# Performance work log

Measured on AMD Instinct MI355X. Metric: run time of the kernel, lower is better.

The kernel has to match this reference:

```python
import jax, jax.numpy as jnp
import numpy as np

T = 512          # tokens
H = 2048         # hidden_size
E = 256          # n_routed_experts (8 groups x 32)
G = 8            # tucker groups
EPG = 32         # experts per group
K = 6            # top_k
I = 1408         # moe_intermediate_size
R1 = 128         # tucker input rank
R2 = 128         # tucker output rank


def setup_inputs() -> dict:
    key = jax.random.key(0)
    ks = jax.random.split(key, 12)
    s = 0.02
    return {
        "hidden_states": jax.random.normal(ks[0], (T, H), jnp.float32),
        "w_router": jax.random.normal(ks[1], (H, E), jnp.float32) * s,
        # gate_proj Tucker factors: H -> I
        "U_in_gate": jax.random.normal(ks[2], (G, H, R1), jnp.float32) * s,
        "core_gate": jax.random.normal(ks[3], (E, R1, R2), jnp.float32) * s,
        "U_out_gate": jax.random.normal(ks[4], (G, I, R2), jnp.float32) * s,
        # up_proj Tucker factors: H -> I
        "U_in_up": jax.random.normal(ks[5], (G, H, R1), jnp.float32) * s,
        "core_up": jax.random.normal(ks[6], (E, R1, R2), jnp.float32) * s,
        "U_out_up": jax.random.normal(ks[7], (G, I, R2), jnp.float32) * s,
        # down_proj Tucker factors: I -> H
        "U_in_down": jax.random.normal(ks[8], (G, I, R1), jnp.float32) * s,
        "core_down": jax.random.normal(ks[9], (E, R1, R2), jnp.float32) * s,
        "U_out_down": jax.random.normal(ks[10], (G, H, R2), jnp.float32) * s,
    }


def _tucker_apply(x, g, e, U_in, core, U_out):
    """Per-expert Tucker linear: y_t = ((x_t @ U_in[g_t]) @ core[e_t]) @ U_out[g_t].T
    x: [Td, din]; g: [Td] group ids; e: [Td] full expert ids.
    U_in: [G, din, r1]; core: [E, r1, r2]; U_out: [G, dout, r2]."""
    h1 = jnp.einsum('td,gdr->tgr', x, U_in)                       # [Td, G, r1]
    h1 = jnp.take_along_axis(h1, g[:, None, None], axis=1)[:, 0]  # [Td, r1]
    h2 = jnp.einsum('tr,trs->ts', h1, core[e])                    # [Td, r2]
    y = jnp.einsum('ts,gds->tgd', h2, U_out)                      # [Td, G, dout]
    return jnp.take_along_axis(y, g[:, None, None], axis=1)[:, 0]


def reference(hidden_states, w_router, U_in_gate, core_gate, U_out_gate,
              U_in_up, core_up, U_out_up, U_in_down, core_down, U_out_down):
    n_tok, hid = hidden_states.shape
    router_logits = hidden_states @ w_router                          # [T, E]
    probs = jax.nn.softmax(router_logits.astype(jnp.float32), axis=-1)
    routing_weights, selected = jax.lax.top_k(probs, K)               # [T, K]
    routing_weights = routing_weights / routing_weights.sum(-1, keepdims=True)
    routing_weights = routing_weights.astype(hidden_states.dtype)

    xd = jnp.repeat(hidden_states, K, axis=0)                         # [T*K, H]
    e = selected.reshape(-1)                                          # [T*K]
    g = e // EPG                                                      # group ids

    gate_out = _tucker_apply(xd, g, e, U_in_gate, core_gate, U_out_gate)
    up_out = _tucker_apply(xd, g, e, U_in_up, core_up, U_out_up)
    inter = jax.nn.silu(gate_out) * up_out                            # [T*K, I]
    down_out = _tucker_apply(inter, g, e, U_in_down, core_down, U_out_down)

    combined = (down_out.reshape(n_tok, K, hid) * routing_weights[..., None]).sum(axis=1)
    return combined
```

## Files before the change

kernel.cpp:

```cpp
#include <hip/hip_runtime.h>
#include <cmath>
#include <cstdint>

#define TNUM 512
#define HID 2048
#define NEXP 256
#define NGRP 8
#define KTOP 6
#define IDIM 1408
#define RNK 128
#define NPAIR (TNUM*KTOP)
#define NRCAP 3328
#define MAXTILES (NRCAP/32)

typedef _Float16 f16;
typedef f16  f16x8 __attribute__((ext_vector_type(8)));
typedef f16  f16x4 __attribute__((ext_vector_type(4)));
typedef float f32x4 __attribute__((ext_vector_type(4)));
#define MFMA16(a,b,c) __builtin_amdgcn_mfma_f32_16x16x32_f16((a),(b),(c),0,0,0)

static __device__ __forceinline__ float4 ld4(const float* p){ return *reinterpret_cast<const float4*>(p); }
static __device__ __forceinline__ void st4(float* p, float4 v){ *reinterpret_cast<float4*>(p) = v; }
static __device__ __forceinline__ f16x8 ldh8(const f16* p){ return *reinterpret_cast<const f16x8*>(p); }

constexpr size_t A256(size_t x){ return (x + 255) & ~(size_t)255; }
constexpr size_t OFF_SEL    = 0;
constexpr size_t OFF_WT     = A256(OFF_SEL    + (size_t)NPAIR*4);
constexpr size_t OFF_CNT    = A256(OFF_WT     + (size_t)NPAIR*4);
constexpr size_t OFF_ESTART = A256(OFF_CNT    + (size_t)NEXP*4);
constexpr size_t OFF_TG     = A256(OFF_ESTART + (size_t)NEXP*4);
constexpr size_t OFF_HDR    = A256(OFF_TG     + (size_t)MAXTILES*4);
constexpr size_t OFF_ROWT   = A256(OFF_HDR    + 16);
constexpr size_t OFF_POS    = A256(OFF_ROWT   + (size_t)NRCAP*4);
constexpr size_t OFF_BIG    = A256(OFF_POS    + (size_t)NPAIR*4);

constexpr size_t SZ_XH    = (size_t)TNUM*HID*2;
constexpr size_t SZ_UTI   = (size_t)NGRP*RNK*HID*2;
constexpr size_t SZ_CT    = (size_t)NEXP*RNK*RNK*2;
constexpr size_t SZ_H1ALL = (size_t)2*TNUM*NGRP*RNK*2;
constexpr size_t SZ_UO    = (size_t)NGRP*IDIM*RNK*2;
constexpr size_t SZ_UOD   = (size_t)NGRP*HID*RNK*2;
constexpr size_t SZ_WR    = (size_t)NEXP*HID*2;
constexpr size_t SZ_H2    = (size_t)NRCAP*RNK*2;
constexpr size_t SZ_INTER = (size_t)NRCAP*IDIM*2;
constexpr size_t SZ_DOWNO = (size_t)NRCAP*HID*4;

constexpr size_t OFF_XH    = OFF_BIG;
constexpr size_t OFF_XL    = OFF_XH   + SZ_XH;
constexpr size_t OFF_UTIG  = OFF_XL   + SZ_XH;
constexpr size_t OFF_UTIU  = OFF_UTIG + SZ_UTI;
constexpr size_t OFF_CGT   = OFF_UTIU + SZ_UTI;
constexpr size_t OFF_CUT   = OFF_CGT  + SZ_CT;
constexpr size_t OFF_H1    = OFF_CUT  + SZ_CT;
constexpr size_t REG_END   = OFF_H1   + SZ_H1ALL;
constexpr size_t OFF_INTER = OFF_XH;
constexpr size_t OFF_DOWNO = OFF_XH;
constexpr size_t OFF_LPART = OFF_H1;
constexpr size_t OFF_UOG   = REG_END;
constexpr size_t OFF_UOU   = OFF_UOG  + SZ_UO;
constexpr size_t OFF_UTID  = OFF_UOU  + SZ_UO;
constexpr size_t OFF_UOD   = OFF_UTID + SZ_UO;
constexpr size_t OFF_CDT   = OFF_UOD  + SZ_UOD;
constexpr size_t OFF_WRH   = OFF_CDT  + SZ_CT;
constexpr size_t OFF_WRL   = OFF_WRH  + SZ_WR;
constexpr size_t OFF_H2G   = OFF_WRL  + SZ_WR;
constexpr size_t OFF_H2U   = OFF_H2G  + SZ_H2;
constexpr size_t OFF_D1    = OFF_H2U  + SZ_H2;
constexpr size_t OFF_D2    = OFF_D1   + SZ_H2;
constexpr size_t WS_NEED   = OFF_D2   + SZ_H2;
static_assert(OFF_INTER + SZ_INTER <= OFF_CGT, "inter overlay must end before cores");
static_assert(OFF_DOWNO + SZ_DOWNO <= OFF_UOG, "downo overlay must end before persistent tail");

__global__ __launch_bounds__(256) void k_cvt_main(
    const float* __restrict__ x,   const float* __restrict__ Uog,
    const float* __restrict__ Uou, const float* __restrict__ Uod,
    const float* __restrict__ wr,
    f16* __restrict__ xh, f16* __restrict__ xl,
    f16* __restrict__ uog, f16* __restrict__ uou, f16* __restrict__ uod,
    f16* __restrict__ wh, f16* __restrict__ wl,
    int* __restrict__ cnt){
  __shared__ float tile[32][33];
  const int b = blockIdx.x, tid = threadIdx.x;
  if(b < 1024){
    const size_t i = (size_t)b*256 + tid;
    float4 v = ld4(x + i*4);
    f16x4 H, L;
    H[0]=(f16)v.x; L[0]=(f16)(v.x-(float)H[0]);
    H[1]=(f16)v.y; L[1]=(f16)(v.y-(float)H[1]);
    H[2]=(f16)v.z; L[2]=(f16)(v.z-(float)H[2]);
    H[3]=(f16)v.w; L[3]=(f16)(v.w-(float)H[3]);
    *reinterpret_cast<f16x4*>(xh + i*4) = H;
    *reinterpret_cast<f16x4*>(xl + i*4) = L;
    return;
  }
  if(b < 5888){
    const float* in; f16* hi; size_t i;
    if(b < 2432){        in = Uog; hi = uog; i = (size_t)(b-1024)*256 + tid; }
    else if(b < 3840){   in = Uou; hi = uou; i = (size_t)(b-2432)*256 + tid; }
    else {               in = Uod; hi = uod; i = (size_t)(b-3840)*256 + tid; }
    float4 v = ld4(in + i*4);
    f16x4 H;
    H[0]=(f16)(v.x*16.f); H[1]=(f16)(v.y*16.f); H[2]=(f16)(v.z*16.f); H[3]=(f16)(v.w*16.f);
    *reinterpret_cast<f16x4*>(hi + i*4) = H;
    return;
  }
  const int wb = b - 5888;
  if(wb == 0) cnt[tid] = 0;
  const int c0 = (wb & 7)*32, r0 = (wb >> 3)*32;
  { const int r = tid>>3, c4 = (tid&7)*4;
    float4 v = ld4(wr + (size_t)(r0+r)*NEXP + c0 + c4);
    tile[r][c4]=v.x; tile[r][c4+1]=v.y; tile[r][c4+2]=v.z; tile[r][c4+3]=v.w; }
  __syncthreads();
  { const int c = tid>>3, r4 = (tid&7)*4;
    f16x4 H, L;
    #pragma unroll
    for(int k = 0; k < 4; k++){
      float v = tile[r4+k][c]*16.f;
      H[k] = (f16)v; L[k] = (f16)(v - (float)H[k]);
    }
    const size_t o = (size_t)(c0+c)*HID + r0 + r4;
    *reinterpret_cast<f16x4*>(wh + o) = H;
    *reinterpret_cast<f16x4*>(wl + o) = L; }
}

__global__ __launch_bounds__(256) void k_cvt_t(
    const float* __restrict__ Uig, const float* __restrict__ Uiu, const float* __restrict__ Uid,
    const float* __restrict__ cg,  const float* __restrict__ cu,  const float* __restrict__ cd,
    f16* __restrict__ ig, f16* __restrict__ iu, f16* __restrict__ idn,
    f16* __restrict__ cgt, f16* __restrict__ cut, f16* __restrict__ cdt){
  __shared__ float tile[32][33];
  const int b = blockIdx.x, tid = threadIdx.x;
  const float* in; f16* o; int r0, c0, R, OR;
  if(b < 6144){
    const int cx = b & 3, ry = (b>>2) & 63, z = b >> 8;
    const int tensor = z >> 3, g = z & 7;
    if(tensor == 0){ in = Uig; o = ig; R = HID; }
    else if(tensor == 1){ in = Uiu; o = iu; R = HID; }
    else { in = Uid; o = idn; R = IDIM; }
    r0 = ry*32; c0 = cx*32;
    if(r0 >= R) return;
    in += (size_t)g*R*RNK; o += (size_t)g*RNK*R;
    OR = R;
  } else {
    const int cb = b - 6144;
    const int tensor = cb >> 12, rem = cb & 4095, e = rem >> 4;
    if(tensor == 0){ in = cg; o = cgt; }
    else if(tensor == 1){ in = cu; o = cut; }
    else { in = cd; o = cdt; }
    in += (size_t)e*RNK*RNK; o += (size_t)e*RNK*RNK;
    r0 = ((rem>>2)&3)*32; c0 = (rem&3)*32; R = RNK; OR = RNK;
  }
  { const int r = tid>>3, c4 = (tid&7)*4;
    float4 v = ld4(in + (size_t)(r0+r)*RNK + c0 + c4);
    tile[r][c4]=v.x; tile[r][c4+1]=v.y; tile[r][c4+2]=v.z; tile[r][c4+3]=v.w; }
  __syncthreads();
  { const int c = tid>>3, r4 = (tid&7)*4;
    f16x4 H;
    #pragma unroll
    for(int k = 0; k < 4; k++) H[k] = (f16)(tile[r4+k][c]*16.f);
    *reinterpret_cast<f16x4*>(o + (size_t)(c0+c)*OR + r0 + r4) = H; }
}

__global__ __launch_bounds__(256) void k_router_mfma(
    const f16* __restrict__ xh, const f16* __restrict__ xl,
    const f16* __restrict__ wh, const f16* __restrict__ wl,
    float* __restrict__ lpart){
  __shared__ float red[4][32][64];
  const int m = blockIdx.x, ecol = blockIdx.y, kz = blockIdx.z;
  const int tid = threadIdx.x;
  const int wid = tid>>6, lane = tid&63, q = lane>>4, id = lane&15;
  const int r0 = m*32, e0 = ecol*64;
  const int kb = kz*512 + wid*128;
  f32x4 acc[2][4];
  #pragma unroll
  for(int f = 0; f < 2; f++)
    #pragma unroll
    for(int c = 0; c < 4; c++) acc[f][c] = (f32x4){0.f,0.f,0.f,0.f};
  #pragma unroll
  for(int kk = 0; kk < 128; kk += 32){
    const size_t a0 = (size_t)(r0+id)*HID    + kb + kk + q*8;
    const size_t a1 = (size_t)(r0+16+id)*HID + kb + kk + q*8;
    f16x8 ah0 = ldh8(xh + a0), al0 = ldh8(xl + a0);
    f16x8 ah1 = ldh8(xh + a1), al1 = ldh8(xl + a1);
    #pragma unroll
    for(int c = 0; c < 4; c++){
      const size_t bo = (size_t)(e0 + c*16 + id)*HID + kb + kk + q*8;
      f16x8 bh = ldh8(wh + bo);
      f16x8 bl = ldh8(wl + bo);
      acc[0][c] = MFMA16(ah0, bh, acc[0][c]);
      acc[0][c] = MFMA16(ah0, bl, acc[0][c]);
      acc[0][c] = MFMA16(al0, bh, acc[0][c]);
      acc[1][c] = MFMA16(ah1, bh, acc[1][c]);
      acc[1][c] = MFMA16(ah1, bl, acc[1][c]);
      acc[1][c] = MFMA16(al1, bh, acc[1][c]);
    }
  }
  #pragma unroll
  for(int f = 0; f < 2; f++)
    #pragma unroll
    for(int c = 0; c < 4; c++)
      #pragma unroll
      for(int r = 0; r < 4; r++)
        red[wid][f*16 + q*4 + r][c*16 + id] = acc[f][c][r];
  __syncthreads();
  const int row = tid>>3, c8 = (tid&7)*8;
  float o[8];
  #pragma unroll
  for(int j = 0; j < 8; j++)
    o[j] = (red[0][row][c8+j] + red[1][row][c8+j] + red[2][row][c8+j] + red[3][row][c8+j])*0.0625f;
  float* dst = &lpart[((size_t)kz*TNUM + r0 + row)*NEXP + e0 + c8];
  st4(dst,     make_float4(o[0],o[1],o[2],o[3]));
  st4(dst + 4, make_float4(o[4],o[5],o[6],o[7]));
}

__global__ __launch_bounds__(256) void k_topk(const float* __restrict__ lpart,
                                              int* __restrict__ sel,
                                              float* __restrict__ wt,
                                              int* __restrict__ cnt){
  __shared__ float wv[4];
  __shared__ int   wi[4];
  __shared__ float swin[KTOP];
  __shared__ int   iwin[KTOP];
  const int t = blockIdx.x, tid = threadIdx.x;
  const int lane = tid & 63, wid = tid >> 6;
  const size_t base = (size_t)t*NEXP + tid;
  float v = lpart[base] + lpart[base + (size_t)TNUM*NEXP]
          + lpart[base + (size_t)2*TNUM*NEXP] + lpart[base + (size_t)3*TNUM*NEXP];
  for(int k = 0; k < KTOP; k++){
    float cv = v; int ci = tid;
    #pragma unroll
    for(int off = 1; off < 64; off <<= 1){
      float ov = __shfl_xor(cv, off);
      int   oi = __shfl_xor(ci, off);
      if(ov > cv || (ov == cv && oi < ci)){ cv = ov; ci = oi; }
    }
    if(lane == 0){ wv[wid] = cv; wi[wid] = ci; }
    __syncthreads();
    if(tid == 0){
      float bv = wv[0]; int bi = wi[0];
      #pragma unroll
      for(int w2 = 1; w2 < 4; w2++)
        if(wv[w2] > bv || (wv[w2] == bv && wi[w2] < bi)){ bv = wv[w2]; bi = wi[w2]; }
      swin[k] = bv; iwin[k] = bi;
    }
    __syncthreads();
    if(tid == iwin[k]) v = -INFINITY;
  }
  if(tid == 0){
    float mx = swin[0], s = 0.f, ww[KTOP];
    #pragma unroll
    for(int k = 0; k < KTOP; k++){ ww[k] = expf(swin[k]-mx); s += ww[k]; }
    float inv = 1.f/s;
    #pragma unroll
    for(int k = 0; k < KTOP; k++){
      sel[t*KTOP+k] = iwin[k];
      wt[t*KTOP+k]  = ww[k]*inv;
      atomicAdd(&cnt[iwin[k]], 1);
    }
  }
}

__global__ __launch_bounds__(256) void k_meta_scatter(
    const int* __restrict__ cnt, const int* __restrict__ sel,
    int* __restrict__ estart, int* __restrict__ tile_group, int* __restrict__ hdr,
    int* __restrict__ row_t, int* __restrict__ pos_of_pair){
  __shared__ int scnt[256];
  __shared__ int gsum[8];
  __shared__ int g0[9];
  __shared__ int curs[256];
  const int tid = threadIdx.x;
  scnt[tid] = cnt[tid];
  if(tid < 8) gsum[tid] = 0;
  __syncthreads();
  atomicAdd(&gsum[tid>>5], scnt[tid]);
  __syncthreads();
  if(tid == 0){
    int run = 0;
    for(int g = 0; g < 8; g++){ g0[g] = run; run += (gsum[g]+31) & ~31; }
    g0[8] = run; hdr[0] = run>>5; hdr[1] = run;
  }
  __syncthreads();
  int g = tid >> 5, s = g0[g];
  for(int i = (g<<5); i < tid; i++) s += scnt[i];
  estart[tid] = s; curs[tid] = s;
  const int nt = g0[8] >> 5;
  for(int t2 = tid; t2 < MAXTILES; t2 += 256){
    int gg = -1;
    if(t2 < nt){
      for(int g2 = 0; g2 < 8; g2++) if(t2*32 >= g0[g2] && t2*32 < g0[g2+1]) gg = g2;
    }
    tile_group[t2] = gg;
  }
  __syncthreads();
  for(int p = tid; p < NPAIR; p += 256){
    const int e = sel[p];
    const int pos = atomicAdd(&curs[e], 1);
    row_t[pos] = p / KTOP;
    pos_of_pair[p] = pos;
  }
}

__global__ __launch_bounds__(256) void k_mm_stage1(
    const f16* __restrict__ xh,
    const f16* __restrict__ Bg_, const f16* __restrict__ Bu_,
    f16* __restrict__ H1){
  __shared__ float red[4][32][64];
  const int m = blockIdx.x, nt = blockIdx.y;
  const int pu = nt>>4, g = (nt>>1)&7, ch = nt&1;
  const f16* B = (pu ? Bu_ : Bg_) + (size_t)g*RNK*HID + (size_t)ch*64*HID;
  const int tid = threadIdx.x;
  const int wid = tid>>6, lane = tid&63, q = lane>>4, id = lane&15;
  const int kb = wid*512;
  const int r0 = m*32;
  f32x4 acc[2][4];
  #pragma unroll
  for(int f = 0; f < 2; f++)
    #pragma unroll
    for(int c = 0; c < 4; c++) acc[f][c] = (f32x4){0.f,0.f,0.f,0.f};
  #pragma unroll 4
  for(int kk = 0; kk < 512; kk += 32){
    f16x8 a0 = ldh8(xh + (size_t)(r0+id)*HID    + kb + kk + q*8);
    f16x8 a1 = ldh8(xh + (size_t)(r0+16+id)*HID + kb + kk + q*8);
    #pragma unroll
    for(int c = 0; c < 4; c++){
      f16x8 b = ldh8(B + (size_t)(c*16+id)*HID + kb + kk + q*8);
      acc[0][c] = MFMA16(a0, b, acc[0][c]);
      acc[1][c] = MFMA16(a1, b, acc[1][c]);
    }
  }
  #pragma unroll
  for(int f = 0; f < 2; f++)
    #pragma unroll
    for(int c = 0; c < 4; c++)
      #pragma unroll
      for(int r = 0; r < 4; r++)
        red[wid][f*16 + q*4 + r][c*16 + id] = acc[f][c][r];
  __syncthreads();
  f16* out = H1 + (size_t)pu*TNUM*(NGRP*RNK);
  const int row = tid>>3, c8 = (tid&7)*8;
  f16x8 o8;
  #pragma unroll
  for(int j = 0; j < 8; j++)
    o8[j] = (f16)(red[0][row][c8+j] + red[1][row][c8+j] + red[2][row][c8+j] + red[3][row][c8+j]);
  *reinterpret_cast<f16x8*>(&out[(size_t)(r0+row)*(NGRP*RNK) + g*RNK + ch*64 + c8]) = o8;
}

__global__ __launch_bounds__(256) void k_core2(
    const f16* __restrict__ Cg, const f16* __restrict__ Cu,
    const f16* __restrict__ H1,
    const int* __restrict__ estart, const int* __restrict__ cnt,
    const int* __restrict__ row_t,
    f16* __restrict__ h2g, f16* __restrict__ h2u){
  const int e = blockIdx.x, up = blockIdx.y;
  const int n = cnt[e];
  if(n == 0) return;
  const int j0 = estart[e], g = e >> 5;
  const f16* C = (up ? Cu : Cg) + (size_t)e*RNK*RNK;
  const f16* A = H1 + (size_t)up*TNUM*(NGRP*RNK);
  f16* o = up ? h2u : h2g;
  const int tid = threadIdx.x;
  const int wid = tid>>6, lane = tid&63, q = lane>>4, id = lane&15;
  for(int rt = 0; rt*16 < n; rt++){
    const int jrow = j0 + rt*16 + id;
    const int jj = jrow < j0+n ? jrow : j0;
    const f16* arow = A + (size_t)row_t[jj]*(NGRP*RNK) + g*RNK;
    f32x4 acc0 = (f32x4){0.f,0.f,0.f,0.f};
    f32x4 acc1 = (f32x4){0.f,0.f,0.f,0.f};
    #pragma unroll
    for(int kk = 0; kk < RNK; kk += 32){
      f16x8 a = ldh8(arow + kk + q*8);
      f16x8 b0 = ldh8(C + (size_t)(wid*32 + id)*RNK      + kk + q*8);
      f16x8 b1 = ldh8(C + (size_t)(wid*32 + 16 + id)*RNK + kk + q*8);
      acc0 = MFMA16(a, b0, acc0);
      acc1 = MFMA16(a, b1, acc1);
    }
    #pragma unroll
    for(int r = 0; r < 4; r++){
      const int j = j0 + rt*16 + q*4 + r;
      if(j < j0+n){
        o[(size_t)j*RNK + wid*32 + id]      = (f16)acc0[r];
        o[(size_t)j*RNK + wid*32 + 16 + id] = (f16)acc1[r];
      }
    }
  }
}

__global__ __launch_bounds__(128) void k_mm_gateup(
    const f16* __restrict__ Ag, const f16* __restrict__ Au,
    const f16* __restrict__ Bg, const f16* __restrict__ Bu,
    const int* __restrict__ tg,
    f16* __restrict__ inter){
  const int g = tg[blockIdx.x];
  if(g < 0) return;
  const int j0 = blockIdx.x*32;
  const int tid = threadIdx.x;
  const int wid = tid>>6, lane = tid&63, q = lane>>4, id = lane&15;
  const int c0 = blockIdx.y*128 + wid*64;
  const size_t bbase = (size_t)g*IDIM*RNK;
  f32x4 accg[2][4], accu[2][4];
  #pragma unroll
  for(int f = 0; f < 2; f++)
    #pragma unroll
    for(int c = 0; c < 4; c++){ accg[f][c] = (f32x4){0.f,0.f,0.f,0.f}; accu[f][c] = (f32x4){0.f,0.f,0.f,0.f}; }
  #pragma unroll 2
  for(int kk = 0; kk < RNK; kk += 32){
    const size_t a0off = (size_t)(j0+id)*RNK    + kk + q*8;
    const size_t a1off = (size_t)(j0+16+id)*RNK + kk + q*8;
    f16x8 ag0 = ldh8(Ag + a0off), ag1 = ldh8(Ag + a1off);
    f16x8 au0 = ldh8(Au + a0off), au1 = ldh8(Au + a1off);
    #pragma unroll
    for(int c = 0; c < 4; c++){
      const size_t boff = bbase + (size_t)(c0 + c*16 + id)*RNK + kk + q*8;
      f16x8 bg = ldh8(Bg + boff);
      f16x8 bu = ldh8(Bu + boff);
      accg[0][c] = MFMA16(ag0, bg, accg[0][c]);
      accg[1][c] = MFMA16(ag1, bg, accg[1][c]);
      accu[0][c] = MFMA16(au0, bu, accu[0][c]);
      accu[1][c] = MFMA16(au1, bu, accu[1][c]);
    }
  }
  #pragma unroll
  for(int f = 0; f < 2; f++)
    #pragma unroll
    for(int c = 0; c < 4; c++)
      #pragma unroll
      for(int r = 0; r < 4; r++){
        float vg = accg[f][c][r] * (1.f/4096.f);
        float vu = accu[f][c][r] * (1.f/4096.f);
        float sv = vg/(1.f+expf(-vg))*vu*256.f;
        inter[(size_t)(j0 + f*16 + q*4 + r)*IDIM + c0 + c*16 + id] = (f16)sv;
      }
}

__global__ __launch_bounds__(256) void k_mm_down_in(
    const f16* __restrict__ A_, const f16* __restrict__ B_,
    const int* __restrict__ tg,
    f16* __restrict__ d1){
  __shared__ float red[4][32][64];
  const int g = tg[blockIdx.x];
  if(g < 0) return;
  const int j0 = blockIdx.x*32;
  const int ch = blockIdx.y;
  const f16* B = B_ + (size_t)g*RNK*IDIM + (size_t)ch*64*IDIM;
  const int tid = threadIdx.x;
  const int wid = tid>>6, lane = tid&63, q = lane>>4, id = lane&15;
  const int kb = wid*352;
  f32x4 acc[2][4];
  #pragma unroll
  for(int f = 0; f < 2; f++)
    #pragma unroll
    for(int c = 0; c < 4; c++) acc[f][c] = (f32x4){0.f,0.f,0.f,0.f};
  #pragma unroll 2
  for(int kk = 0; kk < 352; kk += 32){
    f16x8 a0 = ldh8(A_ + (size_t)(j0+id)*IDIM    + kb + kk + q*8);
    f16x8 a1 = ldh8(A_ + (size_t)(j0+16+id)*IDIM + kb + kk + q*8);
    #pragma unroll
    for(int c = 0; c < 4; c++){
      f16x8 b = ldh8(B + (size_t)(c*16+id)*IDIM + kb + kk + q*8);
      acc[0][c] = MFMA16(a0, b, acc[0][c]);
      acc[1][c] = MFMA16(a1, b, acc[1][c]);
    }
  }
  #pragma unroll
  for(int f = 0; f < 2; f++)
    #pragma unroll
    for(int c = 0; c < 4; c++)
      #pragma unroll
      for(int r = 0; r < 4; r++)
        red[wid][f*16 + q*4 + r][c*16 + id] = acc[f][c][r];
  __syncthreads();
  const int row = tid>>3, c8 = (tid&7)*8;
  f16x8 o8;
  #pragma unroll
  for(int j = 0; j < 8; j++)
    o8[j] = (f16)(red[0][row][c8+j] + red[1][row][c8+j] + red[2][row][c8+j] + red[3][row][c8+j]);
  *reinterpret_cast<f16x8*>(&d1[(size_t)(j0+row)*RNK + ch*64 + c8]) = o8;
}

__global__ __launch_bounds__(256) void k_core_down(
    const f16* __restrict__ Cd,
    const f16* __restrict__ d1,
    const int* __restrict__ estart, const int* __restrict__ cnt,
    f16* __restrict__ d2){
  const int e = blockIdx.x;
  const int n = cnt[e];
  if(n == 0) return;
  const int j0 = estart[e];
  const f16* C = Cd + (size_t)e*RNK*RNK;
  const int tid = threadIdx.x;
  const int wid = tid>>6, lane = tid&63, q = lane>>4, id = lane&15;
  for(int rt = 0; rt*16 < n; rt++){
    const int jrow = j0 + rt*16 + id;
    const int jj = jrow < j0+n ? jrow : j0;
    const f16* arow = d1 + (size_t)jj*RNK;
    f32x4 acc0 = (f32x4){0.f,0.f,0.f,0.f};
    f32x4 acc1 = (f32x4){0.f,0.f,0.f,0.f};
    #pragma unroll
    for(int kk = 0; kk < RNK; kk += 32){
      f16x8 a = ldh8(arow + kk + q*8);
      f16x8 b0 = ldh8(C + (size_t)(wid*32 + id)*RNK      + kk + q*8);
      f16x8 b1 = ldh8(C + (size_t)(wid*32 + 16 + id)*RNK + kk + q*8);
      acc0 = MFMA16(a, b0, acc0);
      acc1 = MFMA16(a, b1, acc1);
    }
    #pragma unroll
    for(int r = 0; r < 4; r++){
      const int j = j0 + rt*16 + q*4 + r;
      if(j < j0+n){
        d2[(size_t)j*RNK + wid*32 + id]      = (f16)acc0[r];
        d2[(size_t)j*RNK + wid*32 + 16 + id] = (f16)acc1[r];
      }
    }
  }
}

__global__ __launch_bounds__(128) void k_mm_down_out(
    const f16* __restrict__ A_, const f16* __restrict__ B_,
    const int* __restrict__ tg,
    float* __restrict__ downo){
  const int g = tg[blockIdx.x];
  if(g < 0) return;
  const int j0 = blockIdx.x*32;
  const f16* B = B_ + (size_t)g*HID*RNK;
  const int tid = threadIdx.x;
  const int wid = tid>>6, lane = tid&63, q = lane>>4, id = lane&15;
  const int c0 = blockIdx.y*128 + wid*64;
  f32x4 acc[2][4];
  #pragma unroll
  for(int f = 0; f < 2; f++)
    #pragma unroll
    for(int c = 0; c < 4; c++) acc[f][c] = (f32x4){0.f,0.f,0.f,0.f};
  #pragma unroll 2
  for(int kk = 0; kk < RNK; kk += 32){
    f16x8 a0 = ldh8(A_ + (size_t)(j0+id)*RNK    + kk + q*8);
    f16x8 a1 = ldh8(A_ + (size_t)(j0+16+id)*RNK + kk + q*8);
    #pragma unroll
    for(int c = 0; c < 4; c++){
      f16x8 b = ldh8(B + (size_t)(c0 + c*16 + id)*RNK + kk + q*8);
      acc[0][c] = MFMA16(a0, b, acc[0][c]);
      acc[1][c] = MFMA16(a1, b, acc[1][c]);
    }
  }
  #pragma unroll
  for(int f = 0; f < 2; f++)
    #pragma unroll
    for(int c = 0; c < 4; c++)
      #pragma unroll
      for(int r = 0; r < 4; r++)
        downo[(size_t)(j0 + f*16 + q*4 + r)*HID + c0 + c*16 + id] = acc[f][c][r]*(1.f/1048576.f);
}

__global__ __launch_bounds__(256) void k_combine(const float* __restrict__ downo,
                                                 const int* __restrict__ pos_of_pair,
                                                 const float* __restrict__ wt,
                                                 float* __restrict__ out){
  const int idx = blockIdx.x*256 + threadIdx.x;
  const int t  = idx >> 9;
  const int h4 = (idx & 511) << 2;
  float4 acc = make_float4(0.f,0.f,0.f,0.f);
  #pragma unroll
  for(int k = 0; k < KTOP; k++){
    const int p = t*KTOP + k;
    const float w = wt[p];
    const int pos = pos_of_pair[p];
    float4 v = ld4(&downo[(size_t)pos*HID + h4]);
    acc.x += w*v.x; acc.y += w*v.y; acc.z += w*v.z; acc.w += w*v.w;
  }
  st4(&out[(size_t)t*HID + h4], acc);
}

extern "C" void kernel_launch(void* const* d_in, const int* in_sizes, int n_in,
                              void* d_out, int out_size, void* d_ws, size_t ws_size,
                              hipStream_t stream){
  const float* x   = (const float*)d_in[0];
  const float* wr  = (const float*)d_in[1];
  const float* Uig = (const float*)d_in[2];
  const float* cg  = (const float*)d_in[3];
  const float* Uog = (const float*)d_in[4];
  const float* Uiu = (const float*)d_in[5];
  const float* cu  = (const float*)d_in[6];
  const float* Uou = (const float*)d_in[7];
  const float* Uid = (const float*)d_in[8];
  const float* cd  = (const float*)d_in[9];
  const float* Uod = (const float*)d_in[10];
  float* out = (float*)d_out;
  char* ws = (char*)d_ws;
  if(ws_size < WS_NEED) return;

  int*   sel    = (int*)  (ws + OFF_SEL);
  float* wt     = (float*)(ws + OFF_WT);
  int*   cnt    = (int*)  (ws + OFF_CNT);
  int*   estart = (int*)  (ws + OFF_ESTART);
  int*   tg     = (int*)  (ws + OFF_TG);
  int*   hdr    = (int*)  (ws + OFF_HDR);
  int*   row_t  = (int*)  (ws + OFF_ROWT);
  int*   pos    = (int*)  (ws + OFF_POS);
  float* lpart  = (float*)(ws + OFF_LPART);
  f16* xh    = (f16*)(ws + OFF_XH);
  f16* xl    = (f16*)(ws + OFF_XL);
  f16* utig  = (f16*)(ws + OFF_UTIG);
  f16* utiu  = (f16*)(ws + OFF_UTIU);
  f16* cgt   = (f16*)(ws + OFF_CGT);
  f16* cut   = (f16*)(ws + OFF_CUT);
  f16* cdt   = (f16*)(ws + OFF_CDT);
  f16* H1    = (f16*)(ws + OFF_H1);
  f16* uog   = (f16*)(ws + OFF_UOG);
  f16* uou   = (f16*)(ws + OFF_UOU);
  f16* utid  = (f16*)(ws + OFF_UTID);
  f16* uod   = (f16*)(ws + OFF_UOD);
  f16* wrh   = (f16*)(ws + OFF_WRH);
  f16* wrl   = (f16*)(ws + OFF_WRL);
  f16* h2g   = (f16*)(ws + OFF_H2G);
  f16* h2u   = (f16*)(ws + OFF_H2U);
  f16* inter = (f16*)(ws + OFF_INTER);
  f16* d1    = (f16*)(ws + OFF_D1);
  f16* d2    = (f16*)(ws + OFF_D2);
  float* downo = (float*)(ws + OFF_DOWNO);

  k_cvt_main <<<6400,              256, 0, stream>>>(x, Uog, Uou, Uod, wr,
                                                     xh, xl, uog, uou, uod, wrh, wrl, cnt);
  k_cvt_t    <<<18432,             256, 0, stream>>>(Uig, Uiu, Uid, cg, cu, cd,
                                                     utig, utiu, utid, cgt, cut, cdt);

  k_router_mfma<<<dim3(16,4,4),    256, 0, stream>>>(xh, xl, wrh, wrl, lpart);
  k_topk     <<<TNUM,              256, 0, stream>>>(lpart, sel, wt, cnt);
  k_meta_scatter<<<1,              256, 0, stream>>>(cnt, sel, estart, tg, hdr, row_t, pos);

  k_mm_stage1<<<dim3(16,32),       256, 0, stream>>>(xh, utig, utiu, H1);
  k_core2    <<<dim3(NEXP,2),      256, 0, stream>>>(cgt, cut, H1, estart, cnt, row_t, h2g, h2u);
  k_mm_gateup<<<dim3(MAXTILES,11), 128, 0, stream>>>(h2g, h2u, uog, uou, tg, inter);
  k_mm_down_in<<<dim3(MAXTILES,2), 256, 0, stream>>>(inter, utid, tg, d1);
  k_core_down<<<NEXP,              256, 0, stream>>>(cdt, d1, estart, cnt, d2);
  k_mm_down_out<<<dim3(MAXTILES,16),128,0, stream>>>(d2, uod, tg, downo);
  k_combine  <<<1024,              256, 0, stream>>>(downo, pos, wt, out);
}
```

Baseline: 146.1 us.

## Fuse core transposes into consumer kernels, merge converters, store down output in fp16

The separate transpose-and-convert pass over the three core tensors is removed. k_core2 and k_core_down now read the fp32 core of their expert directly and transpose it into LDS, and the remaining conversions are merged into a single launch. The down-projection output is stored in fp16 with a 1/1024 rescale folded into the combine weights, which halves that intermediate's traffic. The stage-1 grid axes are also swapped to change block ordering. In exchange the core kernels take an extra per-block prologue, and the fp16 intermediate output carries some risk of precision loss or overflow.

```diff
diff --git a/kernel.cpp b/kernel.cpp
--- a/kernel.cpp
+++ b/kernel.cpp
@@ -36,22 +36,19 @@
 
 constexpr size_t SZ_XH    = (size_t)TNUM*HID*2;
 constexpr size_t SZ_UTI   = (size_t)NGRP*RNK*HID*2;
-constexpr size_t SZ_CT    = (size_t)NEXP*RNK*RNK*2;
 constexpr size_t SZ_H1ALL = (size_t)2*TNUM*NGRP*RNK*2;
 constexpr size_t SZ_UO    = (size_t)NGRP*IDIM*RNK*2;
 constexpr size_t SZ_UOD   = (size_t)NGRP*HID*RNK*2;
 constexpr size_t SZ_WR    = (size_t)NEXP*HID*2;
 constexpr size_t SZ_H2    = (size_t)NRCAP*RNK*2;
 constexpr size_t SZ_INTER = (size_t)NRCAP*IDIM*2;
-constexpr size_t SZ_DOWNO = (size_t)NRCAP*HID*4;
+constexpr size_t SZ_DOWNO = (size_t)NRCAP*HID*2;
 
 constexpr size_t OFF_XH    = OFF_BIG;
 constexpr size_t OFF_XL    = OFF_XH   + SZ_XH;
 constexpr size_t OFF_UTIG  = OFF_XL   + SZ_XH;
 constexpr size_t OFF_UTIU  = OFF_UTIG + SZ_UTI;
-constexpr size_t OFF_CGT   = OFF_UTIU + SZ_UTI;
-constexpr size_t OFF_CUT   = OFF_CGT  + SZ_CT;
-constexpr size_t OFF_H1    = OFF_CUT  + SZ_CT;
+constexpr size_t OFF_H1    = OFF_UTIU + SZ_UTI;
 constexpr size_t REG_END   = OFF_H1   + SZ_H1ALL;
 constexpr size_t OFF_INTER = OFF_XH;
 constexpr size_t OFF_DOWNO = OFF_XH;
@@ -60,24 +57,26 @@
 constexpr size_t OFF_UOU   = OFF_UOG  + SZ_UO;
 constexpr size_t OFF_UTID  = OFF_UOU  + SZ_UO;
 constexpr size_t OFF_UOD   = OFF_UTID + SZ_UO;
-constexpr size_t OFF_CDT   = OFF_UOD  + SZ_UOD;
-constexpr size_t OFF_WRH   = OFF_CDT  + SZ_CT;
+constexpr size_t OFF_WRH   = OFF_UOD  + SZ_UOD;
 constexpr size_t OFF_WRL   = OFF_WRH  + SZ_WR;
 constexpr size_t OFF_H2G   = OFF_WRL  + SZ_WR;
 constexpr size_t OFF_H2U   = OFF_H2G  + SZ_H2;
 constexpr size_t OFF_D1    = OFF_H2U  + SZ_H2;
 constexpr size_t OFF_D2    = OFF_D1   + SZ_H2;
 constexpr size_t WS_NEED   = OFF_D2   + SZ_H2;
-static_assert(OFF_INTER + SZ_INTER <= OFF_CGT, "inter overlay must end before cores");
+static_assert(OFF_INTER + SZ_INTER <= OFF_H1 + 0*SZ_H1ALL + (OFF_H1-OFF_XH), "inter overlay");
+static_assert(OFF_INTER + SZ_INTER <= OFF_UTIU + SZ_UTI, "inter must end before H1");
 static_assert(OFF_DOWNO + SZ_DOWNO <= OFF_UOG, "downo overlay must end before persistent tail");
 
-__global__ __launch_bounds__(256) void k_cvt_main(
+__global__ __launch_bounds__(256) void k_cvt(
     const float* __restrict__ x,   const float* __restrict__ Uog,
     const float* __restrict__ Uou, const float* __restrict__ Uod,
     const float* __restrict__ wr,
+    const float* __restrict__ Uig, const float* __restrict__ Uiu, const float* __restrict__ Uid,
     f16* __restrict__ xh, f16* __restrict__ xl,
     f16* __restrict__ uog, f16* __restrict__ uou, f16* __restrict__ uod,
     f16* __restrict__ wh, f16* __restrict__ wl,
+    f16* __restrict__ ig, f16* __restrict__ iu, f16* __restrict__ idn,
     int* __restrict__ cnt){
   __shared__ float tile[32][33];
   const int b = blockIdx.x, tid = threadIdx.x;
@@ -104,52 +103,36 @@
     *reinterpret_cast<f16x4*>(hi + i*4) = H;
     return;
   }
-  const int wb = b - 5888;
-  if(wb == 0) cnt[tid] = 0;
-  const int c0 = (wb & 7)*32, r0 = (wb >> 3)*32;
-  { const int r = tid>>3, c4 = (tid&7)*4;
-    float4 v = ld4(wr + (size_t)(r0+r)*NEXP + c0 + c4);
-    tile[r][c4]=v.x; tile[r][c4+1]=v.y; tile[r][c4+2]=v.z; tile[r][c4+3]=v.w; }
-  __syncthreads();
-  { const int c = tid>>3, r4 = (tid&7)*4;
-    f16x4 H, L;
-    #pragma unroll
-    for(int k = 0; k < 4; k++){
-      float v = tile[r4+k][c]*16.f;
-      H[k] = (f16)v; L[k] = (f16)(v - (float)H[k]);
-    }
-    const size_t o = (size_t)(c0+c)*HID + r0 + r4;
-    *reinterpret_cast<f16x4*>(wh + o) = H;
-    *reinterpret_cast<f16x4*>(wl + o) = L; }
-}
-
-__global__ __launch_bounds__(256) void k_cvt_t(
-    const float* __restrict__ Uig, const float* __restrict__ Uiu, const float* __restrict__ Uid,
-    const float* __restrict__ cg,  const float* __restrict__ cu,  const float* __restrict__ cd,
-    f16* __restrict__ ig, f16* __restrict__ iu, f16* __restrict__ idn,
-    f16* __restrict__ cgt, f16* __restrict__ cut, f16* __restrict__ cdt){
-  __shared__ float tile[32][33];
-  const int b = blockIdx.x, tid = threadIdx.x;
-  const float* in; f16* o; int r0, c0, R, OR;
-  if(b < 6144){
-    const int cx = b & 3, ry = (b>>2) & 63, z = b >> 8;
-    const int tensor = z >> 3, g = z & 7;
-    if(tensor == 0){ in = Uig; o = ig; R = HID; }
-    else if(tensor == 1){ in = Uiu; o = iu; R = HID; }
-    else { in = Uid; o = idn; R = IDIM; }
-    r0 = ry*32; c0 = cx*32;
-    if(r0 >= R) return;
-    in += (size_t)g*R*RNK; o += (size_t)g*RNK*R;
-    OR = R;
-  } else {
-    const int cb = b - 6144;
-    const int tensor = cb >> 12, rem = cb & 4095, e = rem >> 4;
-    if(tensor == 0){ in = cg; o = cgt; }
-    else if(tensor == 1){ in = cu; o = cut; }
-    else { in = cd; o = cdt; }
-    in += (size_t)e*RNK*RNK; o += (size_t)e*RNK*RNK;
-    r0 = ((rem>>2)&3)*32; c0 = (rem&3)*32; R = RNK; OR = RNK;
-  }
+  if(b < 6400){
+    const int wb = b - 5888;
+    if(wb == 0) cnt[tid] = 0;
+    const int c0 = (wb & 7)*32, r0 = (wb >> 3)*32;
+    { const int r = tid>>3, c4 = (tid&7)*4;
+      float4 v = ld4(wr + (size_t)(r0+r)*NEXP + c0 + c4);
+      tile[r][c4]=v.x; tile[r][c4+1]=v.y; tile[r][c4+2]=v.z; tile[r][c4+3]=v.w; }
+    __syncthreads();
+    { const int c = tid>>3, r4 = (tid&7)*4;
+      f16x4 H, L;
+      #pragma unroll
+      for(int k = 0; k < 4; k++){
+        float v = tile[r4+k][c]*16.f;
+        H[k] = (f16)v; L[k] = (f16)(v - (float)H[k]);
+      }
+      const size_t o = (size_t)(c0+c)*HID + r0 + r4;
+      *reinterpret_cast<f16x4*>(wh + o) = H;
+      *reinterpret_cast<f16x4*>(wl + o) = L; }
+    return;
+  }
+  const int b2 = b - 6400;
+  const int cx = b2 & 3, ry = (b2>>2) & 63, z = b2 >> 8;
+  const int tensor = z >> 3, g = z & 7;
+  const float* in; f16* o; int R;
+  if(tensor == 0){ in = Uig; o = ig; R = HID; }
+  else if(tensor == 1){ in = Uiu; o = iu; R = HID; }
+  else { in = Uid; o = idn; R = IDIM; }
+  const int r0 = ry*32, c0 = cx*32;
+  if(r0 >= R) return;
+  in += (size_t)g*R*RNK; o += (size_t)g*RNK*R;
   { const int r = tid>>3, c4 = (tid&7)*4;
     float4 v = ld4(in + (size_t)(r0+r)*RNK + c0 + c4);
     tile[r][c4]=v.x; tile[r][c4+1]=v.y; tile[r][c4+2]=v.z; tile[r][c4+3]=v.w; }
@@ -158,7 +141,7 @@
     f16x4 H;
     #pragma unroll
     for(int k = 0; k < 4; k++) H[k] = (f16)(tile[r4+k][c]*16.f);
-    *reinterpret_cast<f16x4*>(o + (size_t)(c0+c)*OR + r0 + r4) = H; }
+    *reinterpret_cast<f16x4*>(o + (size_t)(c0+c)*R + r0 + r4) = H; }
 }
 
 __global__ __launch_bounds__(256) void k_router_mfma(
@@ -305,7 +288,7 @@
     const f16* __restrict__ Bg_, const f16* __restrict__ Bu_,
     f16* __restrict__ H1){
   __shared__ float red[4][32][64];
-  const int m = blockIdx.x, nt = blockIdx.y;
+  const int nt = blockIdx.x, m = blockIdx.y;
   const int pu = nt>>4, g = (nt>>1)&7, ch = nt&1;
   const f16* B = (pu ? Bu_ : Bg_) + (size_t)g*RNK*HID + (size_t)ch*64*HID;
   const int tid = threadIdx.x;
@@ -346,19 +329,35 @@
 }
 
 __global__ __launch_bounds__(256) void k_core2(
-    const f16* __restrict__ Cg, const f16* __restrict__ Cu,
+    const float* __restrict__ Cg, const float* __restrict__ Cu,
     const f16* __restrict__ H1,
     const int* __restrict__ estart, const int* __restrict__ cnt,
     const int* __restrict__ row_t,
     f16* __restrict__ h2g, f16* __restrict__ h2u){
+  __shared__ f16 Cs[RNK][RNK+8];
+  __shared__ float tile[32][33];
   const int e = blockIdx.x, up = blockIdx.y;
   const int n = cnt[e];
   if(n == 0) return;
+  const float* Cf = (up ? Cu : Cg) + (size_t)e*RNK*RNK;
+  const int tid = threadIdx.x;
+  #pragma unroll 2
+  for(int st = 0; st < 16; st++){
+    const int R0 = (st>>2)*32, C0 = (st&3)*32;
+    { const int r = tid>>3, c4 = (tid&7)*4;
+      float4 v = ld4(Cf + (size_t)(R0+r)*RNK + C0 + c4);
+      tile[r][c4]=v.x; tile[r][c4+1]=v.y; tile[r][c4+2]=v.z; tile[r][c4+3]=v.w; }
+    __syncthreads();
+    { const int c = tid>>3, r4 = (tid&7)*4;
+      f16x4 H;
+      #pragma unroll
+      for(int k2 = 0; k2 < 4; k2++) H[k2] = (f16)(tile[r4+k2][c]*16.f);
+      *reinterpret_cast<f16x4*>(&Cs[C0+c][R0+r4]) = H; }
+    __syncthreads();
+  }
   const int j0 = estart[e], g = e >> 5;
-  const f16* C = (up ? Cu : Cg) + (size_t)e*RNK*RNK;
   const f16* A = H1 + (size_t)up*TNUM*(NGRP*RNK);
   f16* o = up ? h2u : h2g;
-  const int tid = threadIdx.x;
   const int wid = tid>>6, lane = tid&63, q = lane>>4, id = lane&15;
   for(int rt = 0; rt*16 < n; rt++){
     const int jrow = j0 + rt*16 + id;
@@ -369,8 +368,8 @@
     #pragma unroll
     for(int kk = 0; kk < RNK; kk += 32){
       f16x8 a = ldh8(arow + kk + q*8);
-      f16x8 b0 = ldh8(C + (size_t)(wid*32 + id)*RNK      + kk + q*8);
-      f16x8 b1 = ldh8(C + (size_t)(wid*32 + 16 + id)*RNK + kk + q*8);
+      f16x8 b0 = *reinterpret_cast<const f16x8*>(&Cs[wid*32 + id][kk + q*8]);
+      f16x8 b1 = *reinterpret_cast<const f16x8*>(&Cs[wid*32 + 16 + id][kk + q*8]);
       acc0 = MFMA16(a, b0, acc0);
       acc1 = MFMA16(a, b1, acc1);
     }
@@ -478,16 +477,32 @@
 }
 
 __global__ __launch_bounds__(256) void k_core_down(
-    const f16* __restrict__ Cd,
+    const float* __restrict__ Cd,
     const f16* __restrict__ d1,
     const int* __restrict__ estart, const int* __restrict__ cnt,
     f16* __restrict__ d2){
+  __shared__ f16 Cs[RNK][RNK+8];
+  __shared__ float tile[32][33];
   const int e = blockIdx.x;
   const int n = cnt[e];
   if(n == 0) return;
+  const float* Cf = Cd + (size_t)e*RNK*RNK;
+  const int tid = threadIdx.x;
+  #pragma unroll 2
+  for(int st = 0; st < 16; st++){
+    const int R0 = (st>>2)*32, C0 = (st&3)*32;
+    { const int r = tid>>3, c4 = (tid&7)*4;
+      float4 v = ld4(Cf + (size_t)(R0+r)*RNK + C0 + c4);
+      tile[r][c4]=v.x; tile[r][c4+1]=v.y; tile[r][c4+2]=v.z; tile[r][c4+3]=v.w; }
+    __syncthreads();
+    { const int c = tid>>3, r4 = (tid&7)*4;
+      f16x4 H;
+      #pragma unroll
+      for(int k2 = 0; k2 < 4; k2++) H[k2] = (f16)(tile[r4+k2][c]*16.f);
+      *reinterpret_cast<f16x4*>(&Cs[C0+c][R0+r4]) = H; }
+    __syncthreads();
+  }
   const int j0 = estart[e];
-  const f16* C = Cd + (size_t)e*RNK*RNK;
-  const int tid = threadIdx.x;
   const int wid = tid>>6, lane = tid&63, q = lane>>4, id = lane&15;
   for(int rt = 0; rt*16 < n; rt++){
     const int jrow = j0 + rt*16 + id;
@@ -498,8 +513,8 @@
     #pragma unroll
     for(int kk = 0; kk < RNK; kk += 32){
       f16x8 a = ldh8(arow + kk + q*8);
-      f16x8 b0 = ldh8(C + (size_t)(wid*32 + id)*RNK      + kk + q*8);
-      f16x8 b1 = ldh8(C + (size_t)(wid*32 + 16 + id)*RNK + kk + q*8);
+      f16x8 b0 = *reinterpret_cast<const f16x8*>(&Cs[wid*32 + id][kk + q*8]);
+      f16x8 b1 = *reinterpret_cast<const f16x8*>(&Cs[wid*32 + 16 + id][kk + q*8]);
       acc0 = MFMA16(a, b0, acc0);
       acc1 = MFMA16(a, b1, acc1);
     }
@@ -517,7 +532,7 @@
 __global__ __launch_bounds__(128) void k_mm_down_out(
     const f16* __restrict__ A_, const f16* __restrict__ B_,
     const int* __restrict__ tg,
-    float* __restrict__ downo){
+    f16* __restrict__ downo){
   const int g = tg[blockIdx.x];
   if(g < 0) return;
   const int j0 = blockIdx.x*32;
@@ -547,10 +562,10 @@
     for(int c = 0; c < 4; c++)
       #pragma unroll
       for(int r = 0; r < 4; r++)
-        downo[(size_t)(j0 + f*16 + q*4 + r)*HID + c0 + c*16 + id] = acc[f][c][r]*(1.f/1048576.f);
-}
-
-__global__ __launch_bounds__(256) void k_combine(const float* __restrict__ downo,
+        downo[(size_t)(j0 + f*16 + q*4 + r)*HID + c0 + c*16 + id] = (f16)(acc[f][c][r]*(1.f/1024.f));
+}
+
+__global__ __launch_bounds__(256) void k_combine(const f16* __restrict__ downo,
                                                  const int* __restrict__ pos_of_pair,
                                                  const float* __restrict__ wt,
                                                  float* __restrict__ out){
@@ -561,10 +576,11 @@
   #pragma unroll
   for(int k = 0; k < KTOP; k++){
     const int p = t*KTOP + k;
-    const float w = wt[p];
+    const float w = wt[p]*(1.f/1024.f);
     const int pos = pos_of_pair[p];
-    float4 v = ld4(&downo[(size_t)pos*HID + h4]);
-    acc.x += w*v.x; acc.y += w*v.y; acc.z += w*v.z; acc.w += w*v.w;
+    f16x4 v = *reinterpret_cast<const f16x4*>(&downo[(size_t)pos*HID + h4]);
+    acc.x += w*(float)v[0]; acc.y += w*(float)v[1];
+    acc.z += w*(float)v[2]; acc.w += w*(float)v[3];
   }
   st4(&out[(size_t)t*HID + h4], acc);
 }
@@ -600,9 +616,6 @@
   f16* xl    = (f16*)(ws + OFF_XL);
   f16* utig  = (f16*)(ws + OFF_UTIG);
   f16* utiu  = (f16*)(ws + OFF_UTIU);
-  f16* cgt   = (f16*)(ws + OFF_CGT);
-  f16* cut   = (f16*)(ws + OFF_CUT);
-  f16* cdt   = (f16*)(ws + OFF_CDT);
   f16* H1    = (f16*)(ws + OFF_H1);
   f16* uog   = (f16*)(ws + OFF_UOG);
   f16* uou   = (f16*)(ws + OFF_UOU);
@@ -615,22 +628,21 @@
   f16* inter = (f16*)(ws + OFF_INTER);
   f16* d1    = (f16*)(ws + OFF_D1);
   f16* d2    = (f16*)(ws + OFF_D2);
-  float* downo = (float*)(ws + OFF_DOWNO);
-
-  k_cvt_main <<<6400,              256, 0, stream>>>(x, Uog, Uou, Uod, wr,
-                                                     xh, xl, uog, uou, uod, wrh, wrl, cnt);
-  k_cvt_t    <<<18432,             256, 0, stream>>>(Uig, Uiu, Uid, cg, cu, cd,
-                                                     utig, utiu, utid, cgt, cut, cdt);
+  f16* downo = (f16*)(ws + OFF_DOWNO);
+
+  k_cvt      <<<12544,             256, 0, stream>>>(x, Uog, Uou, Uod, wr, Uig, Uiu, Uid,
+                                                     xh, xl, uog, uou, uod, wrh, wrl,
+                                                     utig, utiu, utid, cnt);
 
   k_router_mfma<<<dim3(16,4,4),    256, 0, stream>>>(xh, xl, wrh, wrl, lpart);
   k_topk     <<<TNUM,              256, 0, stream>>>(lpart, sel, wt, cnt);
   k_meta_scatter<<<1,              256, 0, stream>>>(cnt, sel, estart, tg, hdr, row_t, pos);
 
-  k_mm_stage1<<<dim3(16,32),       256, 0, stream>>>(xh, utig, utiu, H1);
-  k_core2    <<<dim3(NEXP,2),      256, 0, stream>>>(cgt, cut, H1, estart, cnt, row_t, h2g, h2u);
+  k_mm_stage1<<<dim3(32,16),       256, 0, stream>>>(xh, utig, utiu, H1);
+  k_core2    <<<dim3(NEXP,2),      256, 0, stream>>>(cg, cu, H1, estart, cnt, row_t, h2g, h2u);
   k_mm_gateup<<<dim3(MAXTILES,11), 128, 0, stream>>>(h2g, h2u, uog, uou, tg, inter);
   k_mm_down_in<<<dim3(MAXTILES,2), 256, 0, stream>>>(inter, utid, tg, d1);
-  k_core_down<<<NEXP,              256, 0, stream>>>(cdt, d1, estart, cnt, d2);
+  k_core_down<<<NEXP,              256, 0, stream>>>(cd, d1, estart, cnt, d2);
   k_mm_down_out<<<dim3(MAXTILES,16),128,0, stream>>>(d2, uod, tg, downo);
   k_combine  <<<1024,              256, 0, stream>>>(downo, pos, wt, out);
 }
```

After: 145.6 us. No clear change (-0.4%).
